# Performance work log

Measured on AMD Instinct MI355X. Metric: run time of the kernel, lower is better.

Reference implementation:

```python
import jax, jax.numpy as jnp
import numpy as np
import itertools

# ---- module hyperparams (from args) ----
B = 4
H, W = 480, 640                 # frame_height, frame_width
NSEM = 16                       # num_sem_categories
RES = 5                         # map_resolution (cm/cell)
ZRES = 5
MAP_CM = 4800 // 2              # map_size_cm // global_downscaling
M = MAP_CM // RES               # local map cells = 480
VR = 100                        # vision_range
FOV = 79.0                      # hfov degrees
DU_SCALE = 1
CAT_THR, EXP_THR, MAP_THR = 5.0, 1.0, 1.0
AGENT_H = 0.88 * 100.0          # camera_height * 100 (cm)
MAX_H = int(360 / ZRES)         # 72
MIN_H = int(-40 / ZRES)         # -8
NZ = MAX_H - MIN_H              # 80 height bins
C = 4 + NSEM                    # obs channels
RAD2DEG = 57.29577951308232


def setup_inputs():
    key = jax.random.key(0)
    k1, k2, k3, k4 = jax.random.split(key, 4)
    obs = jax.random.uniform(k1, (B, C, H, W), dtype=jnp.float32)
    obs = obs.at[:, 3].multiply(500.0)  # depth channel in cm
    pose_obs = jax.random.normal(k2, (B, 3), dtype=jnp.float32) * 0.1
    maps_last = jax.random.uniform(k3, (B, C, M, M), dtype=jnp.float32)
    poses_last = jax.random.normal(k4, (B, 3), dtype=jnp.float32)
    return {"obs": obs, "pose_obs": pose_obs, "maps_last": maps_last, "poses_last": poses_last}


def _point_cloud(depth):
    # du.get_point_cloud_from_z_t; depth: (B,H,W) cm -> (B,H,W,3)
    f = (W / 2.0) / np.tan(np.deg2rad(FOV / 2.0))
    xc, zc = (W - 1) / 2.0, (H - 1) / 2.0
    gx = jnp.arange(W, dtype=jnp.float32)[None, None, :]
    gz = jnp.arange(H - 1, -1, -1, dtype=jnp.float32)[None, :, None]
    X = (gx - xc) * depth / f
    Z = (gz - zc) * depth / f
    return jnp.stack([X, depth, Z], axis=-1)


def _splat_feat_nd(dims, feat, coords):
    # du.splat_feat_nd: trilinear scatter-splat of per-point feats into dense grid.
    # feat: (B,F,N), coords: (B,3,N) normalized to [-1,1]. Returns (B,F,*dims).
    Bn, Fc, N = feat.shape
    pos = [coords[:, d] * (dims[d] / 2.0) + dims[d] / 2.0 for d in range(3)]
    idxs, wtss = [], []
    for offs in itertools.product((0, 1), repeat=3):
        index = jnp.zeros_like(pos[0])
        wts = jnp.ones_like(pos[0])
        for d in range(3):
            p = jnp.floor(pos[d]) + offs[d]
            safe = ((p > 0) & (p < dims[d])).astype(jnp.float32)
            wts = wts * (1.0 - jnp.abs(pos[d] - p)) * safe
            index = index * dims[d] + p * safe
        idxs.append(index)
        wtss.append(wts)
    idx = jnp.concatenate(idxs, -1).astype(jnp.int32)       # (B, 8N)
    wts = jnp.concatenate(wtss, -1)                         # (B, 8N)
    vals = jnp.tile(feat, (1, 1, 8)) * wts[:, None, :]      # (B, F, 8N)
    ncell = dims[0] * dims[1] * dims[2]
    grid = jax.vmap(lambda i, v: jnp.zeros((Fc, ncell), jnp.float32).at[:, i].add(v))(idx, vals)
    return jnp.round(grid).reshape(Bn, Fc, *dims)


def _affine_grid(theta, Hh, Ww):
    # F.affine_grid, align_corners=True. theta: (B,2,3) -> (B,Hh,Ww,2)
    xs = jnp.linspace(-1.0, 1.0, Ww)
    ys = jnp.linspace(-1.0, 1.0, Hh)
    gy, gx = jnp.meshgrid(ys, xs, indexing="ij")
    base = jnp.stack([gx, gy, jnp.ones_like(gx)], -1)       # (Hh,Ww,3)
    return jnp.einsum("hwk,bjk->bhwj", base, theta)


def _grid_sample(img, grid):
    # F.grid_sample bilinear, zeros padding, align_corners=True.
    Bn, Cc, Hi, Wi = img.shape
    x = (grid[..., 0] + 1.0) * 0.5 * (Wi - 1)
    y = (grid[..., 1] + 1.0) * 0.5 * (Hi - 1)
    x0 = jnp.floor(x); y0 = jnp.floor(y)
    x1, y1 = x0 + 1, y0 + 1

    def gather(ix, iy):
        valid = (ix >= 0) & (ix <= Wi - 1) & (iy >= 0) & (iy <= Hi - 1)
        ixc = jnp.clip(ix, 0, Wi - 1).astype(jnp.int32)
        iyc = jnp.clip(iy, 0, Hi - 1).astype(jnp.int32)
        v = jax.vmap(lambda im, yy, xx: im[:, yy, xx])(img, iyc, ixc)  # (B,C,Hg,Wg)
        return v * valid[:, None].astype(img.dtype)

    wa = (x1 - x) * (y1 - y); wb = (x1 - x) * (y - y0)
    wc = (x - x0) * (y1 - y); wd = (x - x0) * (y - y0)
    return (gather(x0, y0) * wa[:, None] + gather(x0, y1) * wb[:, None]
            + gather(x1, y0) * wc[:, None] + gather(x1, y1) * wd[:, None])


def _forward(obs, pose_obs, maps_last, poses_last):
    depth = obs[:, 3]
    pc = _point_cloud(depth)                                # camera frame (cm)
    # transform_camera_view_t with elevation 0 deg: rotation = identity, z += agent height
    av = pc.at[..., 2].add(AGENT_H)
    # transform_pose_t with shift_loc=(vr*res//2, 0, pi/2): rot angle = pi/2-pi/2 = 0, x += shift
    avc = av.at[..., 0].add(VR * RES // 2)
    xy = avc[..., :2] / RES
    xy = (xy - VR // 2.0) / VR * 2.0
    z = avc[..., 2] / ZRES
    z = (z - (MAX_H + MIN_H) // 2.0) / (MAX_H - MIN_H) * 2.0
    coords = jnp.concatenate([xy, z[..., None]], -1)        # (B,H,W,3) in [-1,1]
    coords = coords.reshape(B, H * W, 3).transpose(0, 2, 1)  # (B,3,N)
    # feat: ones occupancy channel + avg-pooled(du_scale) semantic channels
    hs, ws = H // DU_SCALE, W // DU_SCALE
    sem = obs[:, 4:4 + NSEM].reshape(B, NSEM, hs, DU_SCALE, ws, DU_SCALE).mean((3, 5))
    feat = jnp.concatenate([jnp.ones((B, 1, hs * ws), jnp.float32),
                            sem.reshape(B, NSEM, hs * ws)], 1)
    voxels = _splat_feat_nd((VR, VR, NZ), feat, coords)
    voxels = jnp.swapaxes(voxels, 2, 3)                     # .transpose(2, 3)
    min_z = int(25 / ZRES - MIN_H)                          # 13
    max_z = int((AGENT_H + 1) / ZRES - MIN_H)               # 25
    agent_height_proj = voxels[..., min_z:max_z].sum(-1)
    all_height_proj = voxels.sum(-1)
    fp_map_pred = jnp.clip(agent_height_proj[:, 0:1] / MAP_THR, 0.0, 1.0)
    fp_exp_pred = jnp.clip(all_height_proj[:, 0:1] / EXP_THR, 0.0, 1.0)
    agent_view = jnp.zeros((B, C, M, M), jnp.float32)
    x1 = M // 2 - VR // 2; x2 = x1 + VR
    y1 = M // 2; y2 = y1 + VR
    agent_view = agent_view.at[:, 0:1, y1:y2, x1:x2].set(fp_map_pred)
    agent_view = agent_view.at[:, 1:2, y1:y2, x1:x2].set(fp_exp_pred)
    agent_view = agent_view.at[:, 4:, y1:y2, x1:x2].set(
        jnp.clip(agent_height_proj[:, 1:] / CAT_THR, 0.0, 1.0))
    # get_new_pose_batch (uses pre-update theta for x/y, then wraps theta)
    r = poses_last[:, 2] / RAD2DEG
    yy = poses_last[:, 1] + pose_obs[:, 0] * jnp.sin(r) + pose_obs[:, 1] * jnp.cos(r)
    xx = poses_last[:, 0] + pose_obs[:, 0] * jnp.cos(r) - pose_obs[:, 1] * jnp.sin(r)
    oo = poses_last[:, 2] + pose_obs[:, 2] * RAD2DEG
    oo = jnp.fmod(oo - 180.0, 360.0) + 180.0
    oo = jnp.fmod(oo + 180.0, 360.0) - 180.0
    current_poses = jnp.stack([xx, yy, oo], 1)
    st = jax.lax.stop_gradient(current_poses)               # .clone().detach()
    st_xy = -(st[:, :2] * 100.0 / RES - M // 2) / (M // 2)
    st_t = (90.0 - st[:, 2]) * np.pi / 180.0
    cos_t, sin_t = jnp.cos(st_t), jnp.sin(st_t)
    zero = jnp.zeros_like(cos_t); one = jnp.ones_like(cos_t)
    theta1 = jnp.stack([jnp.stack([cos_t, -sin_t, zero], 1),
                        jnp.stack([sin_t, cos_t, zero], 1)], 1)
    theta2 = jnp.stack([jnp.stack([one, zero, st_xy[:, 0]], 1),
                        jnp.stack([zero, one, st_xy[:, 1]], 1)], 1)
    rotated = _grid_sample(agent_view, _affine_grid(theta1, M, M))
    translated = _grid_sample(rotated, _affine_grid(theta2, M, M))
    map_pred = jnp.maximum(maps_last, translated)           # max over stacked maps
    return fp_map_pred, map_pred, current_poses


def reference(obs, pose_obs, maps_last, poses_last):
    return _forward(obs, pose_obs, maps_last, poses_last)
```

## Files before the change

### kernel.cpp

```cpp
#include <hip/hip_runtime.h>
#include <math.h>

#define NB 4
#define NC 20
#define NH 480
#define NW 640
#define NPIX (NH*NW)
#define NM 480
#define NVR 100
#define NNZ 80
#define ZLO 13
#define ZHI 25
#define NZB 12
#define NSEM_ 16
#define NBINS 101
#define SREC_CAP 655360

#define WS_HIST     0
#define WS_HIST2    2048
#define WS_STARTS   4096
#define WS_STARTS2  6144
#define WS_CURS     8192
#define WS_CURS2    10240
#define WS_PARAMS   12288
#define WS_RECS     16384
#define WS_PROJ     (WS_RECS + 19660800)
#define WS_SGEOM    (WS_PROJ + 3200000)
#define WS_SSEM     (WS_SGEOM + SREC_CAP*16)
#define WS_FAST_END (WS_SSEM + (size_t)SREC_CAP*64)

__device__ __forceinline__ float p1_chain(float d) {
  float xy1 = d / 5.0f;
  xy1 = (xy1 - 50.0f) / 100.0f * 2.0f;
  return xy1 * 50.0f + 50.0f;
}
__device__ __forceinline__ void p02_chain(float d, int row, int col, float foc,
                                          float& p0, float& p2) {
  float X = ((float)col - 319.5f) * d / foc;
  float Z = ((float)(479 - row) - 239.5f) * d / foc;
  float xy0 = (X + 250.0f) / 5.0f;
  xy0 = (xy0 - 50.0f) / 100.0f * 2.0f;
  float zz = (Z + 88.0f) / 5.0f;
  zz = (zz - 32.0f) / 80.0f * 2.0f;
  p0 = xy0 * 50.0f + 50.0f;
  p2 = zz * 40.0f + 40.0f;
}
__device__ __forceinline__ bool band_ok(float p0, float p2) {
  return (p0 > 0.0f) && (p0 < 100.0f) &&
         (p2 > (float)(ZLO - 1)) && (p2 < (float)ZHI);
}

__global__ __launch_bounds__(64) void pose_kernel(
    const float* __restrict__ pose_obs, const float* __restrict__ poses_last,
    float* __restrict__ out_poses, float* __restrict__ params)
{
  int b = threadIdx.x;
  if (b >= NB) return;
  const float R2D = 57.29577951308232f;
  float plx = poses_last[b*3+0], ply = poses_last[b*3+1], plo = poses_last[b*3+2];
  float dx = pose_obs[b*3+0], dy = pose_obs[b*3+1], dth = pose_obs[b*3+2];
  float r = plo / R2D;
  float sr = sinf(r), cr = cosf(r);
  float yy = ply + dx*sr + dy*cr;
  float xx = plx + dx*cr - dy*sr;
  float oo = plo + dth*R2D;
  oo = fmodf(oo - 180.0f, 360.0f) + 180.0f;
  oo = fmodf(oo + 180.0f, 360.0f) - 180.0f;
  out_poses[b*3+0] = xx;
  out_poses[b*3+1] = yy;
  out_poses[b*3+2] = oo;
  float tx = -((xx*100.0f/5.0f) - 240.0f) / 240.0f;
  float ty = -((yy*100.0f/5.0f) - 240.0f) / 240.0f;
  float th = ((90.0f - oo) * 3.14159274101257324f) / 180.0f;
  params[b*4+0] = cosf(th);
  params[b*4+1] = sinf(th);
  params[b*4+2] = tx;
  params[b*4+3] = ty;
}

__global__ __launch_bounds__(256) void hist_kernel(
    const float* __restrict__ obs, int* __restrict__ hist, int* __restrict__ hist2,
    float foc)
{
  int b = blockIdx.x / 300, blk = blockIdx.x % 300;
  __shared__ int lh[NBINS], lh2[NBINS];
  for (int i = threadIdx.x; i < NBINS; i += 256) { lh[i] = 0; lh2[i] = 0; }
  __syncthreads();
  int pix0 = (blk*256 + threadIdx.x)*4;
  int row = pix0 / NW;
  int c0 = pix0 - row*NW;
  const float4* dp = (const float4*)(obs + ((size_t)b*NC + 3)*NPIX);
  float4 dv = dp[blk*256 + threadIdx.x];
  float dvv[4] = {dv.x, dv.y, dv.z, dv.w};
  #pragma unroll
  for (int k = 0; k < 4; ++k) {
    float p1 = p1_chain(dvv[k]);
    int y0 = (int)floorf(p1);
    y0 = min(max(y0, 0), 100);
    atomicAdd(&lh[y0], 1);
    float p0, p2;
    p02_chain(dvv[k], row, c0 + k, foc, p0, p2);
    if (band_ok(p0, p2)) atomicAdd(&lh2[y0], 1);
  }
  __syncthreads();
  for (int i = threadIdx.x; i < NBINS; i += 256) {
    if (lh[i])  atomicAdd(&hist[b*NBINS + i],  lh[i]);
    if (lh2[i]) atomicAdd(&hist2[b*NBINS + i], lh2[i]);
  }
}

__global__ __launch_bounds__(512) void scan_kernel(
    const int* __restrict__ hist, const int* __restrict__ hist2,
    int* __restrict__ starts, int* __restrict__ cursors,
    int* __restrict__ starts2, int* __restrict__ cursors2)
{
  __shared__ int lh[NB*NBINS], lh2[NB*NBINS];
  __shared__ int ls[NB*NBINS + 1], ls2[NB*NBINS + 1];
  for (int i = threadIdx.x; i < NB*NBINS; i += 512) { lh[i] = hist[i]; lh2[i] = hist2[i]; }
  __syncthreads();
  if (threadIdx.x == 0) {
    int s = 0;
    for (int i = 0; i < NB*NBINS; ++i) { ls[i] = s; s += lh[i]; }
    ls[NB*NBINS] = s;
  }
  if (threadIdx.x == 1) {
    int s = 0;
    for (int i = 0; i < NB*NBINS; ++i) { ls2[i] = s; s += lh2[i]; }
    ls2[NB*NBINS] = s;
  }
  __syncthreads();
  for (int i = threadIdx.x; i < NB*NBINS + 1; i += 512) {
    starts[i] = ls[i];
    starts2[i] = ls2[i];
    if (i < NB*NBINS) { cursors[i] = ls[i]; cursors2[i] = ls2[i]; }
  }
}

__global__ __launch_bounds__(256) void scatter_kernel(
    const float* __restrict__ obs, int* __restrict__ cursors, int* __restrict__ cursors2,
    float4* __restrict__ recs, float4* __restrict__ sgeom, float4* __restrict__ ssem,
    float foc, int do_band)
{
  int b = blockIdx.x / 300, blk = blockIdx.x % 300;
  __shared__ int lh[NBINS], lbase[NBINS], loff[NBINS];
  __shared__ int lh2[NBINS], lbase2[NBINS], loff2[NBINS];
  for (int i = threadIdx.x; i < NBINS; i += 256) {
    lh[i] = 0; loff[i] = 0; lh2[i] = 0; loff2[i] = 0;
  }
  __syncthreads();
  int pix0 = (blk*256 + threadIdx.x)*4;
  int row = pix0 / NW;
  int c0 = pix0 - row*NW;
  const float4* dp = (const float4*)(obs + ((size_t)b*NC + 3)*NPIX);
  float4 dv = dp[blk*256 + threadIdx.x];
  float dvv[4] = {dv.x, dv.y, dv.z, dv.w};
  float rp0[4], rp1[4], rp2[4]; int rbin[4]; bool rb[4];
  #pragma unroll
  for (int k = 0; k < 4; ++k) {
    float p1 = p1_chain(dvv[k]);
    float p0, p2;
    p02_chain(dvv[k], row, c0 + k, foc, p0, p2);
    rp0[k] = p0; rp1[k] = p1; rp2[k] = p2;
    int y0 = (int)floorf(p1); y0 = min(max(y0, 0), 100);
    rbin[k] = y0;
    atomicAdd(&lh[y0], 1);
    rb[k] = do_band && band_ok(p0, p2);
    if (rb[k]) atomicAdd(&lh2[y0], 1);
  }
  __syncthreads();
  for (int i = threadIdx.x; i < NBINS; i += 256) {
    if (lh[i]  > 0) lbase[i]  = atomicAdd(&cursors[b*NBINS + i],  lh[i]);
    if (lh2[i] > 0) lbase2[i] = atomicAdd(&cursors2[b*NBINS + i], lh2[i]);
  }
  __syncthreads();
  int sidx[4];
  #pragma unroll
  for (int k = 0; k < 4; ++k) {
    int idx = atomicAdd(&loff[rbin[k]], 1);
    recs[lbase[rbin[k]] + idx] =
        make_float4(rp0[k], rp1[k], rp2[k], __int_as_float(pix0 + k));
    sidx[k] = -1;
    if (rb[k]) {
      int j = lbase2[rbin[k]] + atomicAdd(&loff2[rbin[k]], 1);
      if (j < SREC_CAP) sidx[k] = j;
    }
  }
  bool anyb = (sidx[0] >= 0) | (sidx[1] >= 0) | (sidx[2] >= 0) | (sidx[3] >= 0);
  if (anyb) {
    #pragma unroll
    for (int k = 0; k < 4; ++k)
      if (sidx[k] >= 0)
        sgeom[sidx[k]] = make_float4(rp0[k], rp1[k], rp2[k], 0.0f);
    int grp = blk*256 + threadIdx.x;
    const float4* obs4 = (const float4*)obs;
    #pragma unroll
    for (int q = 0; q < 4; ++q) {
      float4 v0 = obs4[(((size_t)b*NC + 4 + 4*q + 0)*NPIX >> 2) + grp];
      float4 v1 = obs4[(((size_t)b*NC + 4 + 4*q + 1)*NPIX >> 2) + grp];
      float4 v2 = obs4[(((size_t)b*NC + 4 + 4*q + 2)*NPIX >> 2) + grp];
      float4 v3 = obs4[(((size_t)b*NC + 4 + 4*q + 3)*NPIX >> 2) + grp];
      float a0[4] = {v0.x, v0.y, v0.z, v0.w};
      float a1[4] = {v1.x, v1.y, v1.z, v1.w};
      float a2[4] = {v2.x, v2.y, v2.z, v2.w};
      float a3[4] = {v3.x, v3.y, v3.z, v3.w};
      #pragma unroll
      for (int k = 0; k < 4; ++k)
        if (sidx[k] >= 0)
          ssem[(size_t)sidx[k]*4 + q] = make_float4(a0[k], a1[k], a2[k], a3[k]);
    }
  }
}

__global__ __launch_bounds__(256) void slab0_kernel(
    const float4* __restrict__ recs, const int* __restrict__ starts,
    float* __restrict__ proj, float* __restrict__ out_fp)
{
  int b = blockIdx.x / NVR, Y = blockIdx.x % NVR;
  __shared__ float g[NVR*81];
  for (int i = threadIdx.x; i < NVR*81; i += 256) g[i] = 0.0f;
  __syncthreads();
  if (Y > 0) {
    int lo = starts[b*NBINS + Y - 1];
    int hi = starts[b*NBINS + Y + 1];
    float Yf = (float)Y;
    for (int i = lo + threadIdx.x; i < hi; i += 256) {
      float4 r = recs[i];
      float wy = 1.0f - fabsf(r.y - Yf);
      if (wy <= 0.0f) continue;
      float p0 = r.x, p2 = r.z;
      float fl0 = floorf(p0), fl2 = floorf(p2);
      #pragma unroll
      for (int xo = 0; xo < 2; ++xo) {
        float px = fl0 + (float)xo;
        if (!(px > 0.0f && px < 100.0f)) continue;
        float wxy = (1.0f - fabsf(p0 - px)) * wy;
        if (wxy <= 0.0f) continue;
        int ix = (int)px;
        #pragma unroll
        for (int zo = 0; zo < 2; ++zo) {
          float pz = fl2 + (float)zo;
          if (!(pz > 0.0f && pz < 80.0f)) continue;
          float w = wxy * (1.0f - fabsf(p2 - pz));
          if (w > 0.0f) atomicAdd(&g[ix*81 + (int)pz], w);
        }
      }
    }
  }
  __syncthreads();
  if (threadIdx.x < NVR) {
    int x = threadIdx.x;
    float s_all = 0.0f, s_ag = 0.0f;
    for (int z = 0; z < NNZ; ++z) {
      float v = rintf(g[x*81 + z]);
      s_all += v;
      if (z >= ZLO && z < ZHI) s_ag += v;
    }
    float fp_map = fminf(fmaxf(s_ag, 0.0f), 1.0f);
    float fp_exp = fminf(fmaxf(s_all, 0.0f), 1.0f);
    size_t pb = (((size_t)b*NC + 0)*NVR + Y)*NVR + x;
    proj[pb] = fp_map;
    proj[pb + NVR*NVR] = fp_exp;
    proj[pb + 2*NVR*NVR] = 0.0f;
    proj[pb + 3*NVR*NVR] = 0.0f;
    out_fp[(size_t)b*NVR*NVR + Y*NVR + x] = fp_map;
  }
}

__global__ __launch_bounds__(256) void slab1f_kernel(
    const float4* __restrict__ sgeom, const float4* __restrict__ ssem,
    const int* __restrict__ starts2, float* __restrict__ proj)
{
  int half = blockIdx.x & 1;
  int t = blockIdx.x >> 1;
  int b = t / NVR, Y = t % NVR;
  __shared__ float g[8*NVR*NZB];
  for (int i = threadIdx.x; i < 8*NVR*NZB; i += 256) g[i] = 0.0f;
  __syncthreads();
  if (Y > 0) {
    int lo = starts2[b*NBINS + Y - 1];
    int hi = starts2[b*NBINS + Y + 1];
    float Yf = (float)Y;
    for (int i = lo + threadIdx.x; i < hi; i += 256) {
      float4 ge = sgeom[i];
      float wy = 1.0f - fabsf(ge.y - Yf);
      if (wy <= 0.0f) continue;
      float p2 = ge.z;
      float fl2 = floorf(p2);
      float wz[2]; int iz[2]; bool any = false;
      #pragma unroll
      for (int zo = 0; zo < 2; ++zo) {
        float pz = fl2 + (float)zo;
        bool v = (pz >= (float)ZLO) && (pz < (float)ZHI);
        float w = v ? (1.0f - fabsf(p2 - pz)) : 0.0f;
        wz[zo] = w; iz[zo] = v ? ((int)pz - ZLO) : 0;
        any = any || (w > 0.0f);
      }
      if (!any) continue;
      float p0 = ge.x;
      float fl0 = floorf(p0);
      float4 s0 = ssem[(size_t)i*4 + half*2];
      float4 s1 = ssem[(size_t)i*4 + half*2 + 1];
      float sem[8] = {s0.x, s0.y, s0.z, s0.w, s1.x, s1.y, s1.z, s1.w};
      #pragma unroll
      for (int xo = 0; xo < 2; ++xo) {
        float px = fl0 + (float)xo;
        if (!(px > 0.0f && px < 100.0f)) continue;
        float wxy = (1.0f - fabsf(p0 - px)) * wy;
        if (wxy <= 0.0f) continue;
        int ix = (int)px;
        #pragma unroll
        for (int zo = 0; zo < 2; ++zo) {
          float w = wxy * wz[zo];
          if (w > 0.0f) {
            int cell = ix*NZB + iz[zo];
            #pragma unroll
            for (int s = 0; s < 8; ++s)
              atomicAdd(&g[s*(NVR*NZB) + cell], w * sem[s]);
          }
        }
      }
    }
  }
  __syncthreads();
  for (int p = threadIdx.x; p < NVR*8; p += 256) {
    int x = p >> 3, s = p & 7;
    float acc = 0.0f;
    #pragma unroll
    for (int z = 0; z < NZB; ++z) acc += rintf(g[s*(NVR*NZB) + x*NZB + z]);
    float val = fminf(fmaxf(acc / 5.0f, 0.0f), 1.0f);
    proj[(((size_t)b*NC + 4 + half*8 + s)*NVR + Y)*NVR + x] = val;
  }
}

__global__ __launch_bounds__(256) void slab1_kernel(
    const float* __restrict__ obs, const float4* __restrict__ recs,
    const int* __restrict__ starts, float* __restrict__ proj)
{
  int half = blockIdx.x & 1;
  int t = blockIdx.x >> 1;
  int b = t / NVR, Y = t % NVR;
  __shared__ float g[NVR*NZB*8];
  for (int i = threadIdx.x; i < NVR*NZB*8; i += 256) g[i] = 0.0f;
  __syncthreads();
  if (Y > 0) {
    int lo = starts[b*NBINS + Y - 1];
    int hi = starts[b*NBINS + Y + 1];
    float Yf = (float)Y;
    const float* sbase = obs + ((size_t)b*NC + 4 + half*8)*NPIX;
    for (int i = lo + threadIdx.x; i < hi; i += 256) {
      float4 r = recs[i];
      float wy = 1.0f - fabsf(r.y - Yf);
      if (wy <= 0.0f) continue;
      float p2 = r.z;
      float fl2 = floorf(p2);
      float wz[2]; int iz[2]; bool any = false;
      #pragma unroll
      for (int zo = 0; zo < 2; ++zo) {
        float pz = fl2 + (float)zo;
        bool v = (pz >= (float)ZLO) && (pz < (float)ZHI);
        float w = v ? (1.0f - fabsf(p2 - pz)) : 0.0f;
        wz[zo] = w; iz[zo] = v ? ((int)pz - ZLO) : 0;
        any = any || (w > 0.0f);
      }
      if (!any) continue;
      float p0 = r.x;
      float fl0 = floorf(p0);
      int pid = __float_as_int(r.w);
      float sem[8];
      #pragma unroll
      for (int s = 0; s < 8; ++s) sem[s] = sbase[(size_t)s*NPIX + pid];
      #pragma unroll
      for (int xo = 0; xo < 2; ++xo) {
        float px = fl0 + (float)xo;
        if (!(px > 0.0f && px < 100.0f)) continue;
        float wxy = (1.0f - fabsf(p0 - px)) * wy;
        if (wxy <= 0.0f) continue;
        int ix = (int)px;
        #pragma unroll
        for (int zo = 0; zo < 2; ++zo) {
          float w = wxy * wz[zo];
          if (w > 0.0f) {
            float* gb = &g[(ix*NZB + iz[zo])*8];
            #pragma unroll
            for (int s = 0; s < 8; ++s) atomicAdd(&gb[s], w * sem[s]);
          }
        }
      }
    }
  }
  __syncthreads();
  for (int p = threadIdx.x; p < NVR*8; p += 256) {
    int x = p >> 3, s = p & 7;
    float acc = 0.0f;
    #pragma unroll
    for (int z = 0; z < NZB; ++z) acc += rintf(g[(x*NZB + z)*8 + s]);
    float val = fminf(fmaxf(acc / 5.0f, 0.0f), 1.0f);
    proj[(((size_t)b*NC + 4 + half*8 + s)*NVR + Y)*NVR + x] = val;
  }
}

__global__ __launch_bounds__(256) void transform_kernel(
    const float* __restrict__ maps_last, const float* __restrict__ proj,
    const float* __restrict__ params, float* __restrict__ d_out)
{
  int tid = blockIdx.x * 256 + threadIdx.x;
  int b = tid / (NM*NM);
  int rem = tid - b*(NM*NM);
  int h = rem / NM;
  int w = rem - h*NM;

  float ct = params[b*4+0];
  float st = params[b*4+1];
  float tx = params[b*4+2];
  float ty = params[b*4+3];

  const float step = 2.0f/479.0f;
  float gx = -1.0f + (float)w * step;
  float gy = -1.0f + (float)h * step;
  float X2 = ((gx + tx) + 1.0f) * 0.5f * 479.0f;
  float Y2 = ((gy + ty) + 1.0f) * 0.5f * 479.0f;
  float x0 = floorf(X2), y0 = floorf(Y2);
  float wox[2] = {(x0 + 1.0f) - X2, X2 - x0};
  float woy[2] = {(y0 + 1.0f) - Y2, Y2 - y0};

  float twt[16];
  int   toff[16];
  int nz = 0;
  #pragma unroll
  for (int oy = 0; oy < 2; ++oy) {
    #pragma unroll
    for (int ox = 0; ox < 2; ++ox) {
      int kb = (oy*2 + ox)*4;
      float cx = x0 + (float)ox;
      float cy = y0 + (float)oy;
      float wo = wox[ox]*woy[oy];
      bool ov = (cx >= 0.0f) && (cx <= 479.0f) && (cy >= 0.0f) && (cy <= 479.0f);
      if (ov) {
        float gxr = -1.0f + cx * step;
        float gyr = -1.0f + cy * step;
        float xr = gxr*ct - gyr*st;
        float yr = gxr*st + gyr*ct;
        float XS = (xr + 1.0f)*0.5f*479.0f;
        float YS = (yr + 1.0f)*0.5f*479.0f;
        float ix0 = floorf(XS), iy0 = floorf(YS);
        float wix[2] = {(ix0+1.0f)-XS, XS-ix0};
        float wiy[2] = {(iy0+1.0f)-YS, YS-iy0};
        #pragma unroll
        for (int qy = 0; qy < 2; ++qy) {
          #pragma unroll
          for (int qx = 0; qx < 2; ++qx) {
            int k = kb + qy*2 + qx;
            float ux = ix0 + (float)qx;
            float vy = iy0 + (float)qy;
            float wv = 0.0f; int off = 0;
            if (ux >= 0.0f && ux <= 479.0f && vy >= 0.0f && vy <= 479.0f) {
              int U = (int)ux, V = (int)vy;
              if (U >= 190 && U < 290 && V >= 240 && V < 340) {
                off = (V - 240)*NVR + (U - 190);
                wv = wo * (wix[qx]*wiy[qy]);
              }
            }
            twt[k] = wv; toff[k] = off;
            nz += (wv != 0.0f) ? 1 : 0;
          }
        }
      } else {
        #pragma unroll
        for (int k = 0; k < 4; ++k) { twt[kb+k] = 0.0f; toff[kb+k] = 0; }
      }
    }
  }

  const float* pbase = proj + (size_t)b*NC*NVR*NVR;
  size_t base_idx = (size_t)b*NC*NM*NM + (size_t)h*NM + w;
  if (nz > 0) {
    #pragma unroll 1
    for (int c = 0; c < NC; ++c) {
      size_t idx = base_idx + (size_t)c*NM*NM;
      float ml = maps_last[idx];
      float val = 0.0f;
      if (c != 2 && c != 3) {
        const float* pc = pbase + (size_t)c*NVR*NVR;
        #pragma unroll
        for (int k = 0; k < 16; ++k) val += twt[k]*pc[toff[k]];
      }
      d_out[40000 + idx] = fmaxf(ml, val);
    }
  } else {
    #pragma unroll 1
    for (int c = 0; c < NC; ++c) {
      size_t idx = base_idx + (size_t)c*NM*NM;
      d_out[40000 + idx] = fmaxf(maps_last[idx], 0.0f);
    }
  }
}

extern "C" void kernel_launch(void* const* d_in, const int* in_sizes, int n_in,
                              void* d_out, int out_size, void* d_ws, size_t ws_size,
                              hipStream_t stream)
{
  const float* obs        = (const float*)d_in[0];
  const float* pose_obs   = (const float*)d_in[1];
  const float* maps_last  = (const float*)d_in[2];
  const float* poses_last = (const float*)d_in[3];
  float* out = (float*)d_out;

  char* ws = (char*)d_ws;
  int*    hist    = (int*)(ws + WS_HIST);
  int*    hist2   = (int*)(ws + WS_HIST2);
  int*    starts  = (int*)(ws + WS_STARTS);
  int*    starts2 = (int*)(ws + WS_STARTS2);
  int*    cursors = (int*)(ws + WS_CURS);
  int*    cursors2= (int*)(ws + WS_CURS2);
  float*  params  = (float*)(ws + WS_PARAMS);
  float4* recs    = (float4*)(ws + WS_RECS);
  float*  proj    = (float*)(ws + WS_PROJ);
  float4* sgeom   = (float4*)(ws + WS_SGEOM);
  float4* ssem    = (float4*)(ws + WS_SSEM);

  const bool fast = ws_size >= (size_t)WS_FAST_END;

  hipMemsetAsync(ws, 0, WS_PARAMS, stream);

  const float foc = (float)(((double)NW) / 2.0 / tan(79.0 * 0.5 * M_PI / 180.0));

  pose_kernel<<<1, 64, 0, stream>>>(pose_obs, poses_last, out + 40000 + 18432000, params);
  hist_kernel<<<NB*300, 256, 0, stream>>>(obs, hist, hist2, foc);
  scan_kernel<<<1, 512, 0, stream>>>(hist, hist2, starts, cursors, starts2, cursors2);
  scatter_kernel<<<NB*300, 256, 0, stream>>>(obs, cursors, cursors2, recs, sgeom, ssem,
                                             foc, fast ? 1 : 0);
  slab0_kernel<<<NB*NVR, 256, 0, stream>>>(recs, starts, proj, out);
  if (fast)
    slab1f_kernel<<<NB*NVR*2, 256, 0, stream>>>(sgeom, ssem, starts2, proj);
  else
    slab1_kernel<<<NB*NVR*2, 256, 0, stream>>>(obs, recs, starts, proj);
  transform_kernel<<<(NB*NM*NM)/256, 256, 0, stream>>>(maps_last, proj, params, out);
}
```

Baseline: 603.6 us.

## Fuse slab kernels into persistent kernel and gather semantics by pixel id

```diff
diff --git a/kernel.cpp b/kernel.cpp
--- a/kernel.cpp
+++ b/kernel.cpp
@@ -15,6 +15,7 @@
 #define NSEM_ 16
 #define NBINS 101
 #define SREC_CAP 655360
+#define SLAB_GRID 300
 
 #define WS_HIST     0
 #define WS_HIST2    2048
@@ -26,8 +27,7 @@
 #define WS_RECS     16384
 #define WS_PROJ     (WS_RECS + 19660800)
 #define WS_SGEOM    (WS_PROJ + 3200000)
-#define WS_SSEM     (WS_SGEOM + SREC_CAP*16)
-#define WS_FAST_END (WS_SSEM + (size_t)SREC_CAP*64)
+#define WS_FAST_END (WS_SGEOM + (size_t)SREC_CAP*16)
 
 __device__ __forceinline__ float p1_chain(float d) {
   float xy1 = d / 5.0f;
@@ -138,7 +138,7 @@
 
 __global__ __launch_bounds__(256) void scatter_kernel(
     const float* __restrict__ obs, int* __restrict__ cursors, int* __restrict__ cursors2,
-    float4* __restrict__ recs, float4* __restrict__ sgeom, float4* __restrict__ ssem,
+    float4* __restrict__ recs, float4* __restrict__ sgeom,
     float foc, int do_band)
 {
   int b = blockIdx.x / 300, blk = blockIdx.x % 300;
@@ -173,40 +173,138 @@
     if (lh2[i] > 0) lbase2[i] = atomicAdd(&cursors2[b*NBINS + i], lh2[i]);
   }
   __syncthreads();
-  int sidx[4];
   #pragma unroll
   for (int k = 0; k < 4; ++k) {
     int idx = atomicAdd(&loff[rbin[k]], 1);
     recs[lbase[rbin[k]] + idx] =
         make_float4(rp0[k], rp1[k], rp2[k], __int_as_float(pix0 + k));
-    sidx[k] = -1;
     if (rb[k]) {
       int j = lbase2[rbin[k]] + atomicAdd(&loff2[rbin[k]], 1);
-      if (j < SREC_CAP) sidx[k] = j;
-    }
-  }
-  bool anyb = (sidx[0] >= 0) | (sidx[1] >= 0) | (sidx[2] >= 0) | (sidx[3] >= 0);
-  if (anyb) {
-    #pragma unroll
-    for (int k = 0; k < 4; ++k)
-      if (sidx[k] >= 0)
-        sgeom[sidx[k]] = make_float4(rp0[k], rp1[k], rp2[k], 0.0f);
-    int grp = blk*256 + threadIdx.x;
-    const float4* obs4 = (const float4*)obs;
-    #pragma unroll
-    for (int q = 0; q < 4; ++q) {
-      float4 v0 = obs4[(((size_t)b*NC + 4 + 4*q + 0)*NPIX >> 2) + grp];
-      float4 v1 = obs4[(((size_t)b*NC + 4 + 4*q + 1)*NPIX >> 2) + grp];
-      float4 v2 = obs4[(((size_t)b*NC + 4 + 4*q + 2)*NPIX >> 2) + grp];
-      float4 v3 = obs4[(((size_t)b*NC + 4 + 4*q + 3)*NPIX >> 2) + grp];
-      float a0[4] = {v0.x, v0.y, v0.z, v0.w};
-      float a1[4] = {v1.x, v1.y, v1.z, v1.w};
-      float a2[4] = {v2.x, v2.y, v2.z, v2.w};
-      float a3[4] = {v3.x, v3.y, v3.z, v3.w};
-      #pragma unroll
-      for (int k = 0; k < 4; ++k)
-        if (sidx[k] >= 0)
-          ssem[(size_t)sidx[k]*4 + q] = make_float4(a0[k], a1[k], a2[k], a3[k]);
+      if (j < SREC_CAP)
+        sgeom[j] = make_float4(rp0[k], rp1[k], rp2[k], __int_as_float(pix0 + k));
+    }
+  }
+}
+
+__global__ __launch_bounds__(256, 4) void slabs_kernel(
+    const float* __restrict__ obs,
+    const float4* __restrict__ recs, const float4* __restrict__ sgeom,
+    const int* __restrict__ starts, const int* __restrict__ starts2,
+    float* __restrict__ proj, float* __restrict__ out_fp)
+{
+  __shared__ float g[9600];
+  for (int t = blockIdx.x; t < 1200; t += SLAB_GRID) {
+    __syncthreads();
+    for (int i = threadIdx.x; i < 9600; i += 256) g[i] = 0.0f;
+    __syncthreads();
+    if (t < 400) {
+      int b = t / NVR, Y = t % NVR;
+      if (Y > 0) {
+        int lo = starts[b*NBINS + Y - 1];
+        int hi = starts[b*NBINS + Y + 1];
+        float Yf = (float)Y;
+        for (int i = lo + threadIdx.x; i < hi; i += 256) {
+          float4 r = recs[i];
+          float wy = 1.0f - fabsf(r.y - Yf);
+          if (wy <= 0.0f) continue;
+          float p0 = r.x, p2 = r.z;
+          float fl0 = floorf(p0), fl2 = floorf(p2);
+          #pragma unroll
+          for (int xo = 0; xo < 2; ++xo) {
+            float px = fl0 + (float)xo;
+            if (!(px > 0.0f && px < 100.0f)) continue;
+            float wxy = (1.0f - fabsf(p0 - px)) * wy;
+            if (wxy <= 0.0f) continue;
+            int ix = (int)px;
+            #pragma unroll
+            for (int zo = 0; zo < 2; ++zo) {
+              float pz = fl2 + (float)zo;
+              if (!(pz > 0.0f && pz < 80.0f)) continue;
+              float w = wxy * (1.0f - fabsf(p2 - pz));
+              if (w > 0.0f) atomicAdd(&g[ix*81 + (int)pz], w);
+            }
+          }
+        }
+      }
+      __syncthreads();
+      if (threadIdx.x < NVR) {
+        int x = threadIdx.x;
+        float s_all = 0.0f, s_ag = 0.0f;
+        for (int z = 0; z < NNZ; ++z) {
+          float v = rintf(g[x*81 + z]);
+          s_all += v;
+          if (z >= ZLO && z < ZHI) s_ag += v;
+        }
+        float fp_map = fminf(fmaxf(s_ag, 0.0f), 1.0f);
+        float fp_exp = fminf(fmaxf(s_all, 0.0f), 1.0f);
+        size_t pb = (((size_t)b*NC + 0)*NVR + Y)*NVR + x;
+        proj[pb] = fp_map;
+        proj[pb + NVR*NVR] = fp_exp;
+        proj[pb + 2*NVR*NVR] = 0.0f;
+        proj[pb + 3*NVR*NVR] = 0.0f;
+        out_fp[(size_t)b*NVR*NVR + Y*NVR + x] = fp_map;
+      }
+    } else {
+      int tt = t - 400;
+      int half = tt & 1;
+      int by = tt >> 1;
+      int b = by / NVR, Y = by % NVR;
+      const float* sbase = obs + ((size_t)b*NC + 4 + half*8)*NPIX;
+      if (Y > 0) {
+        int lo = starts2[b*NBINS + Y - 1];
+        int hi = starts2[b*NBINS + Y + 1];
+        float Yf = (float)Y;
+        for (int i = lo + threadIdx.x; i < hi; i += 256) {
+          float4 r = sgeom[i];
+          float wy = 1.0f - fabsf(r.y - Yf);
+          if (wy <= 0.0f) continue;
+          float p2 = r.z;
+          float fl2 = floorf(p2);
+          float wz[2]; int iz[2]; bool any = false;
+          #pragma unroll
+          for (int zo = 0; zo < 2; ++zo) {
+            float pz = fl2 + (float)zo;
+            bool v = (pz >= (float)ZLO) && (pz < (float)ZHI);
+            float w = v ? (1.0f - fabsf(p2 - pz)) : 0.0f;
+            wz[zo] = w; iz[zo] = v ? ((int)pz - ZLO) : 0;
+            any = any || (w > 0.0f);
+          }
+          if (!any) continue;
+          float p0 = r.x;
+          float fl0 = floorf(p0);
+          int pid = __float_as_int(r.w);
+          float sem[8];
+          #pragma unroll
+          for (int s = 0; s < 8; ++s) sem[s] = sbase[(size_t)s*NPIX + pid];
+          #pragma unroll
+          for (int xo = 0; xo < 2; ++xo) {
+            float px = fl0 + (float)xo;
+            if (!(px > 0.0f && px < 100.0f)) continue;
+            float wxy = (1.0f - fabsf(p0 - px)) * wy;
+            if (wxy <= 0.0f) continue;
+            int ix = (int)px;
+            #pragma unroll
+            for (int zo = 0; zo < 2; ++zo) {
+              float w = wxy * wz[zo];
+              if (w > 0.0f) {
+                int cell = ix*NZB + iz[zo];
+                #pragma unroll
+                for (int s = 0; s < 8; ++s)
+                  atomicAdd(&g[s*1200 + cell], w * sem[s]);
+              }
+            }
+          }
+        }
+      }
+      __syncthreads();
+      for (int p = threadIdx.x; p < NVR*8; p += 256) {
+        int x = p >> 3, s = p & 7;
+        float acc = 0.0f;
+        #pragma unroll
+        for (int z = 0; z < NZB; ++z) acc += rintf(g[s*1200 + x*NZB + z]);
+        float val = fminf(fmaxf(acc / 5.0f, 0.0f), 1.0f);
+        proj[(((size_t)b*NC + 4 + half*8 + s)*NVR + Y)*NVR + x] = val;
+      }
     }
   }
 }
@@ -263,72 +361,6 @@
     proj[pb + 2*NVR*NVR] = 0.0f;
     proj[pb + 3*NVR*NVR] = 0.0f;
     out_fp[(size_t)b*NVR*NVR + Y*NVR + x] = fp_map;
-  }
-}
-
-__global__ __launch_bounds__(256) void slab1f_kernel(
-    const float4* __restrict__ sgeom, const float4* __restrict__ ssem,
-    const int* __restrict__ starts2, float* __restrict__ proj)
-{
-  int half = blockIdx.x & 1;
-  int t = blockIdx.x >> 1;
-  int b = t / NVR, Y = t % NVR;
-  __shared__ float g[8*NVR*NZB];
-  for (int i = threadIdx.x; i < 8*NVR*NZB; i += 256) g[i] = 0.0f;
-  __syncthreads();
-  if (Y > 0) {
-    int lo = starts2[b*NBINS + Y - 1];
-    int hi = starts2[b*NBINS + Y + 1];
-    float Yf = (float)Y;
-    for (int i = lo + threadIdx.x; i < hi; i += 256) {
-      float4 ge = sgeom[i];
-      float wy = 1.0f - fabsf(ge.y - Yf);
-      if (wy <= 0.0f) continue;
-      float p2 = ge.z;
-      float fl2 = floorf(p2);
-      float wz[2]; int iz[2]; bool any = false;
-      #pragma unroll
-      for (int zo = 0; zo < 2; ++zo) {
-        float pz = fl2 + (float)zo;
-        bool v = (pz >= (float)ZLO) && (pz < (float)ZHI);
-        float w = v ? (1.0f - fabsf(p2 - pz)) : 0.0f;
-        wz[zo] = w; iz[zo] = v ? ((int)pz - ZLO) : 0;
-        any = any || (w > 0.0f);
-      }
-      if (!any) continue;
-      float p0 = ge.x;
-      float fl0 = floorf(p0);
-      float4 s0 = ssem[(size_t)i*4 + half*2];
-      float4 s1 = ssem[(size_t)i*4 + half*2 + 1];
-      float sem[8] = {s0.x, s0.y, s0.z, s0.w, s1.x, s1.y, s1.z, s1.w};
-      #pragma unroll
-      for (int xo = 0; xo < 2; ++xo) {
-        float px = fl0 + (float)xo;
-        if (!(px > 0.0f && px < 100.0f)) continue;
-        float wxy = (1.0f - fabsf(p0 - px)) * wy;
-        if (wxy <= 0.0f) continue;
-        int ix = (int)px;
-        #pragma unroll
-        for (int zo = 0; zo < 2; ++zo) {
-          float w = wxy * wz[zo];
-          if (w > 0.0f) {
-            int cell = ix*NZB + iz[zo];
-            #pragma unroll
-            for (int s = 0; s < 8; ++s)
-              atomicAdd(&g[s*(NVR*NZB) + cell], w * sem[s]);
-          }
-        }
-      }
-    }
-  }
-  __syncthreads();
-  for (int p = threadIdx.x; p < NVR*8; p += 256) {
-    int x = p >> 3, s = p & 7;
-    float acc = 0.0f;
-    #pragma unroll
-    for (int z = 0; z < NZB; ++z) acc += rintf(g[s*(NVR*NZB) + x*NZB + z]);
-    float val = fminf(fmaxf(acc / 5.0f, 0.0f), 1.0f);
-    proj[(((size_t)b*NC + 4 + half*8 + s)*NVR + Y)*NVR + x] = val;
   }
 }
 
@@ -516,7 +548,6 @@
   float4* recs    = (float4*)(ws + WS_RECS);
   float*  proj    = (float*)(ws + WS_PROJ);
   float4* sgeom   = (float4*)(ws + WS_SGEOM);
-  float4* ssem    = (float4*)(ws + WS_SSEM);
 
   const bool fast = ws_size >= (size_t)WS_FAST_END;
 
@@ -527,12 +558,14 @@
   pose_kernel<<<1, 64, 0, stream>>>(pose_obs, poses_last, out + 40000 + 18432000, params);
   hist_kernel<<<NB*300, 256, 0, stream>>>(obs, hist, hist2, foc);
   scan_kernel<<<1, 512, 0, stream>>>(hist, hist2, starts, cursors, starts2, cursors2);
-  scatter_kernel<<<NB*300, 256, 0, stream>>>(obs, cursors, cursors2, recs, sgeom, ssem,
+  scatter_kernel<<<NB*300, 256, 0, stream>>>(obs, cursors, cursors2, recs, sgeom,
                                              foc, fast ? 1 : 0);
-  slab0_kernel<<<NB*NVR, 256, 0, stream>>>(recs, starts, proj, out);
-  if (fast)
-    slab1f_kernel<<<NB*NVR*2, 256, 0, stream>>>(sgeom, ssem, starts2, proj);
-  else
+  if (fast) {
+    slabs_kernel<<<SLAB_GRID, 256, 0, stream>>>(obs, recs, sgeom, starts, starts2,
+                                                proj, out);
+  } else {
+    slab0_kernel<<<NB*NVR, 256, 0, stream>>>(recs, starts, proj, out);
     slab1_kernel<<<NB*NVR*2, 256, 0, stream>>>(obs, recs, starts, proj);
+  }
   transform_kernel<<<(NB*NM*NM)/256, 256, 0, stream>>>(maps_last, proj, params, out);
 }
```

New measurement: 625.8 us. 3.7% more time.

## Transpose semantic channels to pixel-major and merge slab1 halves into one pass

Applied to the files above, without the earlier changes.

```diff
diff --git a/kernel.cpp b/kernel.cpp
--- a/kernel.cpp
+++ b/kernel.cpp
@@ -14,7 +14,7 @@
 #define NZB 12
 #define NSEM_ 16
 #define NBINS 101
-#define SREC_CAP 655360
+#define SREC_CAP 1048576
 
 #define WS_HIST     0
 #define WS_HIST2    2048
@@ -26,8 +26,8 @@
 #define WS_RECS     16384
 #define WS_PROJ     (WS_RECS + 19660800)
 #define WS_SGEOM    (WS_PROJ + 3200000)
-#define WS_SSEM     (WS_SGEOM + SREC_CAP*16)
-#define WS_FAST_END (WS_SSEM + (size_t)SREC_CAP*64)
+#define WS_SEMT     (WS_SGEOM + (size_t)SREC_CAP*16)
+#define WS_FAST_END (WS_SEMT + (size_t)NB*NPIX*16*4)
 
 __device__ __forceinline__ float p1_chain(float d) {
   float xy1 = d / 5.0f;
@@ -78,6 +78,22 @@
   params[b*4+3] = ty;
 }
 
+__global__ __launch_bounds__(256) void semt_kernel(
+    const float* __restrict__ obs, float* __restrict__ semT)
+{
+  int b = blockIdx.x / 1200, blk = blockIdx.x % 1200;
+  int p = blk*256 + threadIdx.x;
+  const float* src = obs + ((size_t)b*NC + 4)*NPIX + p;
+  float v[16];
+  #pragma unroll
+  for (int s = 0; s < 16; ++s) v[s] = src[(size_t)s*NPIX];
+  float4* dst = (float4*)(semT + ((size_t)b*NPIX + p)*16);
+  dst[0] = make_float4(v[0],  v[1],  v[2],  v[3]);
+  dst[1] = make_float4(v[4],  v[5],  v[6],  v[7]);
+  dst[2] = make_float4(v[8],  v[9],  v[10], v[11]);
+  dst[3] = make_float4(v[12], v[13], v[14], v[15]);
+}
+
 __global__ __launch_bounds__(256) void hist_kernel(
     const float* __restrict__ obs, int* __restrict__ hist, int* __restrict__ hist2,
     float foc)
@@ -138,7 +154,7 @@
 
 __global__ __launch_bounds__(256) void scatter_kernel(
     const float* __restrict__ obs, int* __restrict__ cursors, int* __restrict__ cursors2,
-    float4* __restrict__ recs, float4* __restrict__ sgeom, float4* __restrict__ ssem,
+    float4* __restrict__ recs, float4* __restrict__ sgeom,
     float foc, int do_band)
 {
   int b = blockIdx.x / 300, blk = blockIdx.x % 300;
@@ -173,45 +189,20 @@
     if (lh2[i] > 0) lbase2[i] = atomicAdd(&cursors2[b*NBINS + i], lh2[i]);
   }
   __syncthreads();
-  int sidx[4];
   #pragma unroll
   for (int k = 0; k < 4; ++k) {
     int idx = atomicAdd(&loff[rbin[k]], 1);
     recs[lbase[rbin[k]] + idx] =
         make_float4(rp0[k], rp1[k], rp2[k], __int_as_float(pix0 + k));
-    sidx[k] = -1;
     if (rb[k]) {
       int j = lbase2[rbin[k]] + atomicAdd(&loff2[rbin[k]], 1);
-      if (j < SREC_CAP) sidx[k] = j;
-    }
-  }
-  bool anyb = (sidx[0] >= 0) | (sidx[1] >= 0) | (sidx[2] >= 0) | (sidx[3] >= 0);
-  if (anyb) {
-    #pragma unroll
-    for (int k = 0; k < 4; ++k)
-      if (sidx[k] >= 0)
-        sgeom[sidx[k]] = make_float4(rp0[k], rp1[k], rp2[k], 0.0f);
-    int grp = blk*256 + threadIdx.x;
-    const float4* obs4 = (const float4*)obs;
-    #pragma unroll
-    for (int q = 0; q < 4; ++q) {
-      float4 v0 = obs4[(((size_t)b*NC + 4 + 4*q + 0)*NPIX >> 2) + grp];
-      float4 v1 = obs4[(((size_t)b*NC + 4 + 4*q + 1)*NPIX >> 2) + grp];
-      float4 v2 = obs4[(((size_t)b*NC + 4 + 4*q + 2)*NPIX >> 2) + grp];
-      float4 v3 = obs4[(((size_t)b*NC + 4 + 4*q + 3)*NPIX >> 2) + grp];
-      float a0[4] = {v0.x, v0.y, v0.z, v0.w};
-      float a1[4] = {v1.x, v1.y, v1.z, v1.w};
-      float a2[4] = {v2.x, v2.y, v2.z, v2.w};
-      float a3[4] = {v3.x, v3.y, v3.z, v3.w};
-      #pragma unroll
-      for (int k = 0; k < 4; ++k)
-        if (sidx[k] >= 0)
-          ssem[(size_t)sidx[k]*4 + q] = make_float4(a0[k], a1[k], a2[k], a3[k]);
-    }
-  }
-}
-
-__global__ __launch_bounds__(256) void slab0_kernel(
+      if (j < SREC_CAP)
+        sgeom[j] = make_float4(rp0[k], rp1[k], rp2[k], __int_as_float(pix0 + k));
+    }
+  }
+}
+
+__global__ __launch_bounds__(256) void slab0f_kernel(
     const float4* __restrict__ recs, const int* __restrict__ starts,
     float* __restrict__ proj, float* __restrict__ out_fp)
 {
@@ -223,25 +214,34 @@
     int lo = starts[b*NBINS + Y - 1];
     int hi = starts[b*NBINS + Y + 1];
     float Yf = (float)Y;
-    for (int i = lo + threadIdx.x; i < hi; i += 256) {
-      float4 r = recs[i];
-      float wy = 1.0f - fabsf(r.y - Yf);
-      if (wy <= 0.0f) continue;
-      float p0 = r.x, p2 = r.z;
-      float fl0 = floorf(p0), fl2 = floorf(p2);
-      #pragma unroll
-      for (int xo = 0; xo < 2; ++xo) {
-        float px = fl0 + (float)xo;
-        if (!(px > 0.0f && px < 100.0f)) continue;
-        float wxy = (1.0f - fabsf(p0 - px)) * wy;
-        if (wxy <= 0.0f) continue;
-        int ix = (int)px;
+    for (int i = lo + threadIdx.x; i < hi; i += 1024) {
+      float4 rr[4];
+      #pragma unroll
+      for (int k = 0; k < 4; ++k) {
+        int j = i + k*256;
+        rr[k] = (j < hi) ? recs[j] : make_float4(0.0f, -1.0e9f, 0.0f, 0.0f);
+      }
+      #pragma unroll
+      for (int k = 0; k < 4; ++k) {
+        float4 r = rr[k];
+        float wy = 1.0f - fabsf(r.y - Yf);
+        if (wy <= 0.0f) continue;
+        float p0 = r.x, p2 = r.z;
+        float fl0 = floorf(p0), fl2 = floorf(p2);
         #pragma unroll
-        for (int zo = 0; zo < 2; ++zo) {
-          float pz = fl2 + (float)zo;
-          if (!(pz > 0.0f && pz < 80.0f)) continue;
-          float w = wxy * (1.0f - fabsf(p2 - pz));
-          if (w > 0.0f) atomicAdd(&g[ix*81 + (int)pz], w);
+        for (int xo = 0; xo < 2; ++xo) {
+          float px = fl0 + (float)xo;
+          if (!(px > 0.0f && px < 100.0f)) continue;
+          float wxy = (1.0f - fabsf(p0 - px)) * wy;
+          if (wxy <= 0.0f) continue;
+          int ix = (int)px;
+          #pragma unroll
+          for (int zo = 0; zo < 2; ++zo) {
+            float pz = fl2 + (float)zo;
+            if (!(pz > 0.0f && pz < 80.0f)) continue;
+            float w = wxy * (1.0f - fabsf(p2 - pz));
+            if (w > 0.0f) atomicAdd(&g[ix*81 + (int)pz], w);
+          }
         }
       }
     }
@@ -266,69 +266,88 @@
   }
 }
 
-__global__ __launch_bounds__(256) void slab1f_kernel(
-    const float4* __restrict__ sgeom, const float4* __restrict__ ssem,
+__global__ __launch_bounds__(256) void slab1t_kernel(
+    const float* __restrict__ semT, const float4* __restrict__ sgeom,
     const int* __restrict__ starts2, float* __restrict__ proj)
 {
-  int half = blockIdx.x & 1;
-  int t = blockIdx.x >> 1;
-  int b = t / NVR, Y = t % NVR;
-  __shared__ float g[8*NVR*NZB];
-  for (int i = threadIdx.x; i < 8*NVR*NZB; i += 256) g[i] = 0.0f;
+  int b = blockIdx.x / NVR, Y = blockIdx.x % NVR;
+  __shared__ float g[1200*16];
+  for (int i = threadIdx.x; i < 1200*16; i += 256) g[i] = 0.0f;
   __syncthreads();
   if (Y > 0) {
     int lo = starts2[b*NBINS + Y - 1];
     int hi = starts2[b*NBINS + Y + 1];
     float Yf = (float)Y;
-    for (int i = lo + threadIdx.x; i < hi; i += 256) {
-      float4 ge = sgeom[i];
-      float wy = 1.0f - fabsf(ge.y - Yf);
-      if (wy <= 0.0f) continue;
-      float p2 = ge.z;
-      float fl2 = floorf(p2);
-      float wz[2]; int iz[2]; bool any = false;
-      #pragma unroll
-      for (int zo = 0; zo < 2; ++zo) {
-        float pz = fl2 + (float)zo;
-        bool v = (pz >= (float)ZLO) && (pz < (float)ZHI);
-        float w = v ? (1.0f - fabsf(p2 - pz)) : 0.0f;
-        wz[zo] = w; iz[zo] = v ? ((int)pz - ZLO) : 0;
-        any = any || (w > 0.0f);
-      }
-      if (!any) continue;
-      float p0 = ge.x;
-      float fl0 = floorf(p0);
-      float4 s0 = ssem[(size_t)i*4 + half*2];
-      float4 s1 = ssem[(size_t)i*4 + half*2 + 1];
-      float sem[8] = {s0.x, s0.y, s0.z, s0.w, s1.x, s1.y, s1.z, s1.w};
-      #pragma unroll
-      for (int xo = 0; xo < 2; ++xo) {
-        float px = fl0 + (float)xo;
-        if (!(px > 0.0f && px < 100.0f)) continue;
-        float wxy = (1.0f - fabsf(p0 - px)) * wy;
-        if (wxy <= 0.0f) continue;
-        int ix = (int)px;
+    const float4* sT = (const float4*)(semT + (size_t)b*NPIX*16);
+    for (int i = lo + threadIdx.x; i < hi; i += 1024) {
+      float4 rr[4];
+      #pragma unroll
+      for (int k = 0; k < 4; ++k) {
+        int j = i + k*256;
+        rr[k] = (j < hi) ? sgeom[j]
+                         : make_float4(0.0f, -1.0e9f, 0.0f, __int_as_float(0));
+      }
+      float4 sv[4][4];
+      #pragma unroll
+      for (int k = 0; k < 4; ++k) {
+        int pid = __float_as_int(rr[k].w);
+        const float4* p4 = sT + (size_t)pid*4;
+        sv[k][0] = p4[0]; sv[k][1] = p4[1]; sv[k][2] = p4[2]; sv[k][3] = p4[3];
+      }
+      #pragma unroll
+      for (int k = 0; k < 4; ++k) {
+        float4 r = rr[k];
+        float wy = 1.0f - fabsf(r.y - Yf);
+        if (wy <= 0.0f) continue;
+        float p2 = r.z;
+        float fl2 = floorf(p2);
+        float pz0 = fl2, pz1 = fl2 + 1.0f;
+        bool v0 = (pz0 >= (float)ZLO) && (pz0 < (float)ZHI);
+        bool v1 = (pz1 >= (float)ZLO) && (pz1 < (float)ZHI);
+        float wz0 = v0 ? (1.0f - fabsf(p2 - pz0)) : 0.0f;
+        float wz1 = v1 ? (1.0f - fabsf(p2 - pz1)) : 0.0f;
+        int iz0 = v0 ? ((int)pz0 - ZLO) : 0;
+        int iz1 = v1 ? ((int)pz1 - ZLO) : 0;
+        if (wz0 <= 0.0f && wz1 <= 0.0f) continue;
+        float p0 = r.x;
+        float fl0 = floorf(p0);
+        float px0 = fl0, px1 = fl0 + 1.0f;
+        float wx0 = (px0 > 0.0f && px0 < 100.0f) ? (1.0f - fabsf(p0 - px0)) * wy : 0.0f;
+        float wx1 = (px1 > 0.0f && px1 < 100.0f) ? (1.0f - fabsf(p0 - px1)) * wy : 0.0f;
+        int ix0 = (int)px0, ix1 = ix0 + 1;
+        float sem[16] = {sv[k][0].x, sv[k][0].y, sv[k][0].z, sv[k][0].w,
+                         sv[k][1].x, sv[k][1].y, sv[k][1].z, sv[k][1].w,
+                         sv[k][2].x, sv[k][2].y, sv[k][2].z, sv[k][2].w,
+                         sv[k][3].x, sv[k][3].y, sv[k][3].z, sv[k][3].w};
+        float wx[2] = {wx0, wx1};
+        int ixx[2] = {ix0, ix1};
+        float wz[2] = {wz0, wz1};
+        int izz[2] = {iz0, iz1};
         #pragma unroll
-        for (int zo = 0; zo < 2; ++zo) {
-          float w = wxy * wz[zo];
-          if (w > 0.0f) {
-            int cell = ix*NZB + iz[zo];
-            #pragma unroll
-            for (int s = 0; s < 8; ++s)
-              atomicAdd(&g[s*(NVR*NZB) + cell], w * sem[s]);
+        for (int xo = 0; xo < 2; ++xo) {
+          if (wx[xo] <= 0.0f) continue;
+          #pragma unroll
+          for (int zo = 0; zo < 2; ++zo) {
+            float w = wx[xo] * wz[zo];
+            if (w > 0.0f) {
+              int cb = (ixx[xo]*NZB + izz[zo])*16;
+              #pragma unroll
+              for (int s = 0; s < 16; ++s)
+                atomicAdd(&g[cb + s], w * sem[s]);
+            }
           }
         }
       }
     }
   }
   __syncthreads();
-  for (int p = threadIdx.x; p < NVR*8; p += 256) {
-    int x = p >> 3, s = p & 7;
+  for (int p = threadIdx.x; p < NVR*16; p += 256) {
+    int x = p >> 4, s = p & 15;
     float acc = 0.0f;
     #pragma unroll
-    for (int z = 0; z < NZB; ++z) acc += rintf(g[s*(NVR*NZB) + x*NZB + z]);
+    for (int z = 0; z < NZB; ++z) acc += rintf(g[(x*NZB + z)*16 + s]);
     float val = fminf(fmaxf(acc / 5.0f, 0.0f), 1.0f);
-    proj[(((size_t)b*NC + 4 + half*8 + s)*NVR + Y)*NVR + x] = val;
+    proj[(((size_t)b*NC + 4 + s)*NVR + Y)*NVR + x] = val;
   }
 }
 
@@ -516,7 +535,7 @@
   float4* recs    = (float4*)(ws + WS_RECS);
   float*  proj    = (float*)(ws + WS_PROJ);
   float4* sgeom   = (float4*)(ws + WS_SGEOM);
-  float4* ssem    = (float4*)(ws + WS_SSEM);
+  float*  semT    = (float*)(ws + WS_SEMT);
 
   const bool fast = ws_size >= (size_t)WS_FAST_END;
 
@@ -525,13 +544,15 @@
   const float foc = (float)(((double)NW) / 2.0 / tan(79.0 * 0.5 * M_PI / 180.0));
 
   pose_kernel<<<1, 64, 0, stream>>>(pose_obs, poses_last, out + 40000 + 18432000, params);
+  if (fast)
+    semt_kernel<<<NB*1200, 256, 0, stream>>>(obs, semT);
   hist_kernel<<<NB*300, 256, 0, stream>>>(obs, hist, hist2, foc);
   scan_kernel<<<1, 512, 0, stream>>>(hist, hist2, starts, cursors, starts2, cursors2);
-  scatter_kernel<<<NB*300, 256, 0, stream>>>(obs, cursors, cursors2, recs, sgeom, ssem,
+  scatter_kernel<<<NB*300, 256, 0, stream>>>(obs, cursors, cursors2, recs, sgeom,
                                              foc, fast ? 1 : 0);
-  slab0_kernel<<<NB*NVR, 256, 0, stream>>>(recs, starts, proj, out);
+  slab0f_kernel<<<NB*NVR, 256, 0, stream>>>(recs, starts, proj, out);
   if (fast)
-    slab1f_kernel<<<NB*NVR*2, 256, 0, stream>>>(sgeom, ssem, starts2, proj);
+    slab1t_kernel<<<NB*NVR, 256, 0, stream>>>(semT, sgeom, starts2, proj);
   else
     slab1_kernel<<<NB*NVR*2, 256, 0, stream>>>(obs, recs, starts, proj);
   transform_kernel<<<(NB*NM*NM)/256, 256, 0, stream>>>(maps_last, proj, params, out);
```

New measurement: 706.2 us. 1.17x slower.
